# Optimization experiments

Measured on AMD Instinct MI355X. Metric: run time of the kernel, lower is better.

## Reference

```python
import jax, jax.numpy as jnp
import numpy as np

N_NODES = 128
F = 64            # hidden channels (64x0e + 64x1o)
N_RBF = 8
H_R = 64          # radial MLP hidden
L = 2             # num_interactions
R_MAX = 5.0
AVG_NEIGH = 127.0
G_DIM = 16
N_SPECIES = 5

# static fully-connected edge list (no self edges): E = n*(n-1)
_idx = np.arange(N_NODES)
_s, _r = np.meshgrid(_idx, _idx, indexing='ij')
_mask = _s != _r
SENDERS = jnp.asarray(_s[_mask])    # [E]
RECEIVERS = jnp.asarray(_r[_mask])  # [E]


def setup_inputs() -> dict:
    key = jax.random.key(0)
    ks = jax.random.split(key, 12)
    inp = {
        'positions': jax.random.normal(ks[0], (32, N_NODES, 3), jnp.float32),
        'node_features': jax.random.randint(ks[1], (32, N_NODES), 0, N_SPECIES),
        'global_features': jax.random.normal(ks[2], (32, G_DIM), jnp.float32),
        # learned parameters
        'embed': jax.random.normal(ks[3], (N_SPECIES, F), jnp.float32) * 0.1,
        'glob_w': jax.random.normal(ks[4], (G_DIM, F), jnp.float32) * 0.1,
        'rbf_w1': jax.random.normal(ks[5], (L, N_RBF, H_R), jnp.float32) * 0.3,
        'rbf_b1': jnp.zeros((L, H_R), jnp.float32),
        'rbf_w2': jax.random.normal(ks[6], (L, H_R, 3 * F), jnp.float32) * 0.1,
        'ws': jax.random.normal(ks[7], (L, F, F), jnp.float32) * 0.1,
        'wv': jax.random.normal(ks[8], (L, F, F), jnp.float32) * 0.1,
        'wout': jax.random.normal(ks[9], (F,), jnp.float32) * 0.1,
        'final_scaling': jnp.ones((), jnp.float32),
    }
    return inp


def _rbf(d):
    # gaussian radial basis on [0, r_max]
    centers = jnp.linspace(0.0, R_MAX, N_RBF)
    width = R_MAX / N_RBF
    return jnp.exp(-((d[:, None] - centers) ** 2) / (2.0 * width * width))  # [E, N_RBF]


def _single(pos, species, glob, embed, glob_w, rbf_w1, rbf_b1, rbf_w2, ws, wv, wout, final_scaling):
    # graph construction + edge vectors
    edge_vec = pos[RECEIVERS] - pos[SENDERS]                 # [E,3]
    d = jnp.sqrt(jnp.sum(edge_vec ** 2, axis=-1) + 1e-12)   # [E]
    unit = edge_vec / d[:, None]                             # [E,3]
    phi = _rbf(d)                                            # [E,N_RBF]

    # node embedding (species one-hot lookup) conditioned on global features
    s = embed[species] + glob @ glob_w                       # [n,F] scalars
    v = jnp.zeros((N_NODES, F, 3), pos.dtype)                # [n,F,3] vectors

    for l in range(L):
        rw = jax.nn.silu(phi @ rbf_w1[l] + rbf_b1[l]) @ rbf_w2[l]  # [E,3F]
        r1, r2, r3 = jnp.split(rw, 3, axis=-1)               # each [E,F]
        ms = r1 * s[SENDERS]                                 # [E,F]
        mv = r2[..., None] * v[SENDERS] + (r3 * s[SENDERS])[..., None] * unit[:, None, :]  # [E,F,3]
        agg_s = jax.ops.segment_sum(ms, RECEIVERS, num_segments=N_NODES) / AVG_NEIGH
        agg_v = jax.ops.segment_sum(mv, RECEIVERS, num_segments=N_NODES) / AVG_NEIGH
        s = s + agg_s @ ws[l]
        v = v + jnp.einsum('nfd,fg->ngd', agg_v, wv[l])

    out = jnp.einsum('nfd,f->nd', v, wout)                   # equivariant readout [n,3]
    return (out - pos) * final_scaling


def reference(positions, node_features, global_features, embed, glob_w, rbf_w1,
              rbf_b1, rbf_w2, ws, wv, wout, final_scaling):
    fn = lambda p, sp, g: _single(p, sp, g, embed, glob_w, rbf_w1, rbf_b1,
                                  rbf_w2, ws, wv, wout, final_scaling)
    return jax.vmap(fn)(positions, node_features, global_features)
```

## Files before the change

### kernel.cpp

```cpp
#include <hip/hip_runtime.h>
#include <hip/hip_bf16.h>


#define NN 128
#define BB 32
#define FF 64

using f32x4  = __attribute__((ext_vector_type(4))) float;
using short8 = __attribute__((ext_vector_type(8))) short;
using half4  = __attribute__((ext_vector_type(4))) _Float16;

__device__ __forceinline__ unsigned short f2bf(float x) {
    unsigned int u = __float_as_uint(x);
    u += 0x7fff + ((u >> 16) & 1);
    return (unsigned short)(u >> 16);
}
__device__ __forceinline__ unsigned int f2bf_fast32(float x) {
    return (__float_as_uint(x) + 0x8000u) >> 16;
}

__global__ __launch_bounds__(256) void setup_kernel(
    const float* __restrict__ w2,
    const float* __restrict__ ws,
    const float* __restrict__ wv,
    const float* __restrict__ rbf_w1,
    const float* __restrict__ rbf_b1,
    const int* __restrict__ species, const float* __restrict__ glob,
    const float* __restrict__ embed, const float* __restrict__ glob_w,
    short* __restrict__ w2frag,
    float* __restrict__ wT4,
    _Float16* __restrict__ w1A,
    float* __restrict__ s)
{
    const int blk = blockIdx.x;
    if (blk < 192) {
        const int tid = blk * 256 + threadIdx.x;
        const int NFRAG = 24576;
        if (tid < NFRAG) {
            const int e  = tid & 7;
            const int l  = (tid >> 3) & 63;
            const int ks = (tid >> 9) & 1;
            const int q  = tid >> 10;
            const int nt = q % 3;
            const int wv_ = (q / 3) & 3;
            const int layer = q / 12;
            const int col = nt * 64 + wv_ * 16 + (l & 15);
            const int hb  = ks * 32 + (l >> 4) * 8 + e;
            const float val = w2[layer * 64 * 192 + hb * 192 + col] * (1.0f / 127.0f);
            w2frag[tid] = (short)f2bf(val);
        }
        const int tid2 = tid - NFRAG;
        if (tid2 >= 0 && tid2 < 16384) {
            const int c   = tid2 & 3;
            const int g   = (tid2 >> 2) & 63;
            const int ff4 = (tid2 >> 8) & 15;
            const int m   = (tid2 >> 12) & 1;
            const int layer = tid2 >> 13;
            const float* src = (m == 0 ? ws : wv) + layer * 4096;
            wT4[tid2] = src[(ff4 * 4 + c) * 64 + g];
        }
        const int tid3 = tid - NFRAG - 16384;
        if (tid3 >= 0 && tid3 < 2048) {
            const int e  = tid3 & 3;
            const int l  = (tid3 >> 2) & 63;
            const int wv_ = (tid3 >> 8) & 3;
            const int layer = tid3 >> 10;
            const int k = (l >> 4) * 4 + e;
            const int h = wv_ * 16 + (l & 15);
            float val = 0.0f;
            if (k < 8)       val = rbf_w1[layer * 512 + k * 64 + h];
            else if (k == 8) val = rbf_b1[layer * 64 + h];
            w1A[tid3] = (_Float16)val;
        }
    } else {
        const int node = (blk - 192) * 4 + (threadIdx.x >> 6);
        const int b = node >> 7;
        const int f = threadIdx.x & 63;
        const int sp = species[node];
        float acc = embed[sp * FF + f];
#pragma unroll
        for (int k = 0; k < 16; ++k)
            acc = fmaf(glob[b * 16 + k], glob_w[k * FF + f], acc);
        s[node * FF + f] = acc;
    }
}

template<int LAYER>
__global__ __launch_bounds__(256, 4) void msg_kernel(
    const float* __restrict__ pos,
    const float* __restrict__ s_in,
    const float* __restrict__ v_in,
    const half4* __restrict__ w1Abuf,
    const short* __restrict__ w2frag,
    const float* __restrict__ wT4,
    const float* __restrict__ wout,
    const float* __restrict__ scale,
    float* __restrict__ s_out,
    float* __restrict__ v_out,
    float* __restrict__ out)
{
    __shared__ unsigned short hid_lds[NN * 64];
    __shared__ float4 unit_lds[NN];
    __shared__ __align__(16) char phi_pool[NN * 32];
    float4 (*agg4)[16] = (float4(*)[16])phi_pool;

    const int blk = blockIdx.x;
    const int xcd = blk & 7;
    const int idx = blk >> 3;
    const int b = xcd * 4 + (idx >> 7);
    const int i = idx & 127;

    const int t = threadIdx.x;
    const int w = t >> 6;
    const int l = t & 63;
    const int node = b * NN + i;
    const float* pb = pos + b * NN * 3;

    short8 bfrag[3][2];
    {
        const short8* wf = (const short8*)w2frag;
#pragma unroll
        for (int nt = 0; nt < 3; ++nt)
#pragma unroll
            for (int ks = 0; ks < 2; ++ks)
                bfrag[nt][ks] = wf[((w * 3 + nt) * 2 + ks) * 64 + l];
    }

    {
        const int j = t & 127;
        const int half = t >> 7;
        const float dx = pb[i * 3 + 0] - pb[j * 3 + 0];
        const float dy = pb[i * 3 + 1] - pb[j * 3 + 1];
        const float dz = pb[i * 3 + 2] - pb[j * 3 + 2];
        const float d2 = fmaf(dx, dx, fmaf(dy, dy, fmaf(dz, dz, 1e-12f)));
        const float inv = __builtin_amdgcn_rsqf(d2);
        const float dd = d2 * inv;
        if (half == 0)
            unit_lds[j] = make_float4(dx * inv, dy * inv, dz * inv, 0.0f);
        const _Float16 zf = (_Float16)0.f;
        half4 ph;
#pragma unroll
        for (int r = 0; r < 4; ++r) {
            const float td = dd - (float)(half * 4 + r) * (5.0f / 7.0f);
            ph[r] = (_Float16)__expf(td * td * -1.28f);
        }
        if (j == i) ph = (half4){zf, zf, zf, zf};
        char* rowp = phi_pool + j * 32;
        const int swz = ((j >> 2) & 3) << 3;
        *(half4*)(rowp + ((half * 8) ^ swz)) = ph;
        if (half == 0) {
            half4 bias = {(j == i) ? zf : (_Float16)1.0f, zf, zf, zf};
            *(half4*)(rowp + (16 ^ swz)) = bias;
        } else {
            *(half4*)(rowp + (24 ^ swz)) = (half4){zf, zf, zf, zf};
        }
    }
    __syncthreads();

    {
        const half4 w1a = w1Abuf[w * 64 + l];
        const int jcol = l & 15;
        const int chunk = (l >> 4) * 8;
        const int hbyte = w * 32 + (l >> 4) * 8;
#pragma unroll
        for (int mt = 0; mt < 8; ++mt) {
            const int j = mt * 16 + jcol;
            const half4 bphi = *(const half4*)(
                phi_pool + j * 32 + (chunk ^ (((j >> 2) & 3) << 3)));
            f32x4 pre = __builtin_amdgcn_mfma_f32_16x16x16f16(
                w1a, bphi, (f32x4){0.f, 0.f, 0.f, 0.f}, 0, 0, 0);
            unsigned int pk[2];
#pragma unroll
            for (int p = 0; p < 2; ++p) {
                float sv[2];
#pragma unroll
                for (int q = 0; q < 2; ++q) {
                    const float z = pre[p * 2 + q];
                    const float ex = __expf(-z);
                    sv[q] = z * __builtin_amdgcn_rcpf(1.0f + ex);
                }
                pk[p] = f2bf_fast32(sv[0]) | (f2bf_fast32(sv[1]) << 16);
            }
            const int byte = j * 128 + (hbyte ^ ((j & 7) << 4));
            *(uint2*)((char*)hid_lds + byte) = make_uint2(pk[0], pk[1]);
        }
    }
    __syncthreads();

    const int f    = w * 16 + (l & 15);
    const int jsub = (l >> 4) * 4;
    const float* sb = s_in + b * NN * FF;
    const float4* vb4 = (LAYER > 0) ? ((const float4*)v_in) + b * NN * FF : nullptr;

    float accs = 0.f, av0 = 0.f, av1 = 0.f, av2 = 0.f;

    float sP[4]; float4 vP[4];
#pragma unroll
    for (int reg = 0; reg < 4; ++reg) {
        const int j = jsub + reg;
        sP[reg] = sb[j * FF + f];
        if (LAYER > 0) vP[reg] = vb4[j * FF + f];
    }

#pragma unroll
    for (int mt = 0; mt < 8; ++mt) {
        const int jA = mt * 16 + (l & 15);
        const int base = jA * 128;
        const int sw = (jA & 7) << 4;
        const short8 a0 = *(const short8*)((const char*)hid_lds + base + (((l >> 4) * 16 +  0) ^ sw));
        const short8 a1 = *(const short8*)((const char*)hid_lds + base + (((l >> 4) * 16 + 64) ^ sw));

        f32x4 c0 = (f32x4){0.f, 0.f, 0.f, 0.f};
        f32x4 c1 = (f32x4){0.f, 0.f, 0.f, 0.f};
        f32x4 c2 = (f32x4){0.f, 0.f, 0.f, 0.f};
        c0 = __builtin_amdgcn_mfma_f32_16x16x32_bf16(a0, bfrag[0][0], c0, 0, 0, 0);
        c0 = __builtin_amdgcn_mfma_f32_16x16x32_bf16(a1, bfrag[0][1], c0, 0, 0, 0);
        c1 = __builtin_amdgcn_mfma_f32_16x16x32_bf16(a0, bfrag[1][0], c1, 0, 0, 0);
        c1 = __builtin_amdgcn_mfma_f32_16x16x32_bf16(a1, bfrag[1][1], c1, 0, 0, 0);
        c2 = __builtin_amdgcn_mfma_f32_16x16x32_bf16(a0, bfrag[2][0], c2, 0, 0, 0);
        c2 = __builtin_amdgcn_mfma_f32_16x16x32_bf16(a1, bfrag[2][1], c2, 0, 0, 0);

        float sN[4]; float4 vN[4];
        if (mt < 7) {
#pragma unroll
            for (int reg = 0; reg < 4; ++reg) {
                const int j = (mt + 1) * 16 + jsub + reg;
                sN[reg] = sb[j * FF + f];
                if (LAYER > 0) vN[reg] = vb4[j * FF + f];
            }
        }

#pragma unroll
        for (int reg = 0; reg < 4; ++reg) {
            const int j  = mt * 16 + jsub + reg;
            const float r1 = c0[reg];
            const float r2 = c1[reg];
            const float r3 = c2[reg];
            const float sj = sP[reg];
            const float r3s = r3 * sj;
            const float4 u = unit_lds[j];
            accs = fmaf(r1, sj, accs);
            av0 = fmaf(r3s, u.x, av0);
            av1 = fmaf(r3s, u.y, av1);
            av2 = fmaf(r3s, u.z, av2);
            if (LAYER > 0) {
                av0 = fmaf(r2, vP[reg].x, av0);
                av1 = fmaf(r2, vP[reg].y, av1);
                av2 = fmaf(r2, vP[reg].z, av2);
            }
        }
#pragma unroll
        for (int reg = 0; reg < 4; ++reg) {
            sP[reg] = sN[reg];
            if (LAYER > 0) vP[reg] = vN[reg];
        }
    }

    accs += __shfl_xor(accs, 16, 64); accs += __shfl_xor(accs, 32, 64);
    av0  += __shfl_xor(av0, 16, 64);  av0  += __shfl_xor(av0, 32, 64);
    av1  += __shfl_xor(av1, 16, 64);  av1  += __shfl_xor(av1, 32, 64);
    av2  += __shfl_xor(av2, 16, 64);  av2  += __shfl_xor(av2, 32, 64);
    if (l < 16) {
        ((float*)agg4)[0 * 64 + f] = accs;
        ((float*)agg4)[1 * 64 + f] = av0;
        ((float*)agg4)[2 * 64 + f] = av1;
        ((float*)agg4)[3 * 64 + f] = av2;
    }
    __syncthreads();

    const int g = l;
    const float4* wv4 = (const float4*)wT4;
    if (LAYER == 0) {
        const int m = (w == 0) ? 0 : 1;
        const int row = (w == 0) ? 0 : w;
        float a = (w == 0) ? s_in[node * FF + g] : 0.0f;
#pragma unroll
        for (int k = 0; k < 16; ++k) {
            const float4 w4 = wv4[(m * 16 + k) * 64 + g];
            const float4 a4 = agg4[row][k];
            a = fmaf(a4.x, w4.x, a); a = fmaf(a4.y, w4.y, a);
            a = fmaf(a4.z, w4.z, a); a = fmaf(a4.w, w4.w, a);
        }
        if (w == 0) s_out[node * FF + g] = a;
        else        v_out[(node * FF + g) * 4 + (w - 1)] = a;
    } else {
        if (w > 0) {
            const int d = w - 1;
            float a = v_in[(node * FF + g) * 4 + d];
#pragma unroll
            for (int k = 0; k < 16; ++k) {
                const float4 w4 = wv4[(16 + k) * 64 + g];
                const float4 a4 = agg4[w][k];
                a = fmaf(a4.x, w4.x, a); a = fmaf(a4.y, w4.y, a);
                a = fmaf(a4.z, w4.z, a); a = fmaf(a4.w, w4.w, a);
            }
            float p = a * wout[g];
#pragma unroll
            for (int off = 1; off < 64; off <<= 1)
                p += __shfl_xor(p, off, 64);
            if (l == 0)
                out[node * 3 + d] = (p - pos[node * 3 + d]) * scale[0];
        }
    }
}

extern "C" void kernel_launch(void* const* d_in, const int* in_sizes, int n_in,
                              void* d_out, int out_size, void* d_ws, size_t ws_size,
                              hipStream_t stream) {
    const float* pos     = (const float*)d_in[0];
    const int*   species = (const int*)  d_in[1];
    const float* glob    = (const float*)d_in[2];
    const float* embed   = (const float*)d_in[3];
    const float* glob_w  = (const float*)d_in[4];
    const float* rbf_w1  = (const float*)d_in[5];
    const float* rbf_b1  = (const float*)d_in[6];
    const float* rbf_w2  = (const float*)d_in[7];
    const float* ws      = (const float*)d_in[8];
    const float* wv      = (const float*)d_in[9];
    const float* wout    = (const float*)d_in[10];
    const float* scale   = (const float*)d_in[11];

    float* wsf = (float*)d_ws;
    float* s0     = wsf;
    float* s1     = wsf + 262144;
    float* v1     = wsf + 524288;
    short* w2frag = (short*)(wsf + 1572864);
    float* wT4    = wsf + 1585152;
    _Float16* w1A = (_Float16*)(wsf + 1601536);
    float* outp = (float*)d_out;

    setup_kernel<<<dim3(192 + BB * NN / 4), 256, 0, stream>>>(
        rbf_w2, ws, wv, rbf_w1, rbf_b1, species, glob, embed, glob_w,
        w2frag, wT4, w1A, s0);

    msg_kernel<0><<<dim3(NN * BB), 256, 0, stream>>>(
        pos, s0, nullptr,
        (const half4*)w1A, w2frag, wT4, wout, scale,
        s1, v1, nullptr);

    msg_kernel<1><<<dim3(NN * BB), 256, 0, stream>>>(
        pos, s1, v1,
        (const half4*)(w1A + 1024), w2frag + 12288, wT4 + 8192, wout, scale,
        nullptr, nullptr, outp);
}
```

Measured before the change: 82.81 us.

## Transpose node feature buffers to feature-major layout and vectorize message accumulation

```diff
diff --git a/kernel.cpp b/kernel.cpp
--- a/kernel.cpp
+++ b/kernel.cpp
@@ -75,13 +75,14 @@
     } else {
         const int node = (blk - 192) * 4 + (threadIdx.x >> 6);
         const int b = node >> 7;
+        const int n = node & 127;
         const int f = threadIdx.x & 63;
         const int sp = species[node];
         float acc = embed[sp * FF + f];
 #pragma unroll
         for (int k = 0; k < 16; ++k)
             acc = fmaf(glob[b * 16 + k], glob_w[k * FF + f], acc);
-        s[node * FF + f] = acc;
+        s[b * 8192 + f * 128 + n] = acc;
     }
 }
 
@@ -100,9 +101,11 @@
     float* __restrict__ out)
 {
     __shared__ unsigned short hid_lds[NN * 64];
-    __shared__ float4 unit_lds[NN];
+    __shared__ __align__(16) float ux_lds[NN];
+    __shared__ __align__(16) float uy_lds[NN];
+    __shared__ __align__(16) float uz_lds[NN];
     __shared__ __align__(16) char phi_pool[NN * 32];
-    float4 (*agg4)[16] = (float4(*)[16])phi_pool;
+    f32x4 (*agg4)[16] = (f32x4(*)[16])phi_pool;
 
     const int blk = blockIdx.x;
     const int xcd = blk & 7;
@@ -113,8 +116,20 @@
     const int t = threadIdx.x;
     const int w = t >> 6;
     const int l = t & 63;
-    const int node = b * NN + i;
     const float* pb = pos + b * NN * 3;
+
+    const int f    = w * 16 + (l & 15);
+    const int jsub = (l >> 4) * 4;
+    const float* sbf = s_in + b * 8192 + f * 128;
+    const float* vbf = (LAYER > 0) ? (v_in + b * 24576 + f * 384) : nullptr;
+
+    f32x4 sP = *(const f32x4*)(sbf + jsub);
+    f32x4 vxP, vyP, vzP;
+    if (LAYER > 0) {
+        vxP = *(const f32x4*)(vbf +   0 + jsub);
+        vyP = *(const f32x4*)(vbf + 128 + jsub);
+        vzP = *(const f32x4*)(vbf + 256 + jsub);
+    }
 
     short8 bfrag[3][2];
     {
@@ -135,8 +150,11 @@
         const float d2 = fmaf(dx, dx, fmaf(dy, dy, fmaf(dz, dz, 1e-12f)));
         const float inv = __builtin_amdgcn_rsqf(d2);
         const float dd = d2 * inv;
-        if (half == 0)
-            unit_lds[j] = make_float4(dx * inv, dy * inv, dz * inv, 0.0f);
+        if (half == 0) {
+            ux_lds[j] = dx * inv;
+            uy_lds[j] = dy * inv;
+            uz_lds[j] = dz * inv;
+        }
         const _Float16 zf = (_Float16)0.f;
         half4 ph;
 #pragma unroll
@@ -187,23 +205,14 @@
     }
     __syncthreads();
 
-    const int f    = w * 16 + (l & 15);
-    const int jsub = (l >> 4) * 4;
-    const float* sb = s_in + b * NN * FF;
-    const float4* vb4 = (LAYER > 0) ? ((const float4*)v_in) + b * NN * FF : nullptr;
-
-    float accs = 0.f, av0 = 0.f, av1 = 0.f, av2 = 0.f;
-
-    float sP[4]; float4 vP[4];
-#pragma unroll
-    for (int reg = 0; reg < 4; ++reg) {
-        const int j = jsub + reg;
-        sP[reg] = sb[j * FF + f];
-        if (LAYER > 0) vP[reg] = vb4[j * FF + f];
-    }
+    f32x4 accs4 = (f32x4){0.f, 0.f, 0.f, 0.f};
+    f32x4 av04  = (f32x4){0.f, 0.f, 0.f, 0.f};
+    f32x4 av14  = (f32x4){0.f, 0.f, 0.f, 0.f};
+    f32x4 av24  = (f32x4){0.f, 0.f, 0.f, 0.f};
 
 #pragma unroll
     for (int mt = 0; mt < 8; ++mt) {
+        const int j0 = mt * 16 + jsub;
         const int jA = mt * 16 + (l & 15);
         const int base = jA * 128;
         const int sw = (jA & 7) << 4;
@@ -220,42 +229,39 @@
         c2 = __builtin_amdgcn_mfma_f32_16x16x32_bf16(a0, bfrag[2][0], c2, 0, 0, 0);
         c2 = __builtin_amdgcn_mfma_f32_16x16x32_bf16(a1, bfrag[2][1], c2, 0, 0, 0);
 
-        float sN[4]; float4 vN[4];
+        f32x4 sN, vxN, vyN, vzN;
         if (mt < 7) {
-#pragma unroll
-            for (int reg = 0; reg < 4; ++reg) {
-                const int j = (mt + 1) * 16 + jsub + reg;
-                sN[reg] = sb[j * FF + f];
-                if (LAYER > 0) vN[reg] = vb4[j * FF + f];
+            sN = *(const f32x4*)(sbf + j0 + 16);
+            if (LAYER > 0) {
+                vxN = *(const f32x4*)(vbf +   0 + j0 + 16);
+                vyN = *(const f32x4*)(vbf + 128 + j0 + 16);
+                vzN = *(const f32x4*)(vbf + 256 + j0 + 16);
             }
         }
 
-#pragma unroll
-        for (int reg = 0; reg < 4; ++reg) {
-            const int j  = mt * 16 + jsub + reg;
-            const float r1 = c0[reg];
-            const float r2 = c1[reg];
-            const float r3 = c2[reg];
-            const float sj = sP[reg];
-            const float r3s = r3 * sj;
-            const float4 u = unit_lds[j];
-            accs = fmaf(r1, sj, accs);
-            av0 = fmaf(r3s, u.x, av0);
-            av1 = fmaf(r3s, u.y, av1);
-            av2 = fmaf(r3s, u.z, av2);
-            if (LAYER > 0) {
-                av0 = fmaf(r2, vP[reg].x, av0);
-                av1 = fmaf(r2, vP[reg].y, av1);
-                av2 = fmaf(r2, vP[reg].z, av2);
-            }
-        }
-#pragma unroll
-        for (int reg = 0; reg < 4; ++reg) {
-            sP[reg] = sN[reg];
-            if (LAYER > 0) vP[reg] = vN[reg];
-        }
-    }
-
+        const f32x4 ux4 = *(const f32x4*)(ux_lds + j0);
+        const f32x4 uy4 = *(const f32x4*)(uy_lds + j0);
+        const f32x4 uz4 = *(const f32x4*)(uz_lds + j0);
+
+        accs4 = accs4 + c0 * sP;
+        const f32x4 r3s = c2 * sP;
+        av04 = av04 + r3s * ux4;
+        av14 = av14 + r3s * uy4;
+        av24 = av24 + r3s * uz4;
+        if (LAYER > 0) {
+            av04 = av04 + c1 * vxP;
+            av14 = av14 + c1 * vyP;
+            av24 = av24 + c1 * vzP;
+        }
+
+        sP = sN;
+        if (LAYER > 0) { vxP = vxN; vyP = vyN; vzP = vzN; }
+    }
+
+    float accs = (accs4[0] + accs4[1]) + (accs4[2] + accs4[3]);
+    float av0  = (av04[0] + av04[1]) + (av04[2] + av04[3]);
+    float av1  = (av14[0] + av14[1]) + (av14[2] + av14[3]);
+    float av2  = (av24[0] + av24[1]) + (av24[2] + av24[3]);
     accs += __shfl_xor(accs, 16, 64); accs += __shfl_xor(accs, 32, 64);
     av0  += __shfl_xor(av0, 16, 64);  av0  += __shfl_xor(av0, 32, 64);
     av1  += __shfl_xor(av1, 16, 64);  av1  += __shfl_xor(av1, 32, 64);
@@ -269,31 +275,31 @@
     __syncthreads();
 
     const int g = l;
-    const float4* wv4 = (const float4*)wT4;
+    const int node = b * NN + i;
+    const f32x4* wv4 = (const f32x4*)wT4;
     if (LAYER == 0) {
         const int m = (w == 0) ? 0 : 1;
         const int row = (w == 0) ? 0 : w;
-        float a = (w == 0) ? s_in[node * FF + g] : 0.0f;
-#pragma unroll
-        for (int k = 0; k < 16; ++k) {
-            const float4 w4 = wv4[(m * 16 + k) * 64 + g];
-            const float4 a4 = agg4[row][k];
-            a = fmaf(a4.x, w4.x, a); a = fmaf(a4.y, w4.y, a);
-            a = fmaf(a4.z, w4.z, a); a = fmaf(a4.w, w4.w, a);
-        }
-        if (w == 0) s_out[node * FF + g] = a;
-        else        v_out[(node * FF + g) * 4 + (w - 1)] = a;
+        f32x4 a4 = (f32x4){0.f, 0.f, 0.f, 0.f};
+#pragma unroll
+        for (int k = 0; k < 16; ++k)
+            a4 = a4 + wv4[(m * 16 + k) * 64 + g] * agg4[row][k];
+        float a = (a4[0] + a4[1]) + (a4[2] + a4[3]);
+        if (w == 0) {
+            a += s_in[b * 8192 + g * 128 + i];
+            s_out[b * 8192 + g * 128 + i] = a;
+        } else {
+            v_out[b * 24576 + g * 384 + (w - 1) * 128 + i] = a;
+        }
     } else {
         if (w > 0) {
             const int d = w - 1;
-            float a = v_in[(node * FF + g) * 4 + d];
-#pragma unroll
-            for (int k = 0; k < 16; ++k) {
-                const float4 w4 = wv4[(16 + k) * 64 + g];
-                const float4 a4 = agg4[w][k];
-                a = fmaf(a4.x, w4.x, a); a = fmaf(a4.y, w4.y, a);
-                a = fmaf(a4.z, w4.z, a); a = fmaf(a4.w, w4.w, a);
-            }
+            f32x4 a4 = (f32x4){0.f, 0.f, 0.f, 0.f};
+#pragma unroll
+            for (int k = 0; k < 16; ++k)
+                a4 = a4 + wv4[(16 + k) * 64 + g] * agg4[w][k];
+            float a = (a4[0] + a4[1]) + (a4[2] + a4[3])
+                    + v_in[b * 24576 + g * 384 + d * 128 + i];
             float p = a * wout[g];
 #pragma unroll
             for (int off = 1; off < 64; off <<= 1)
@@ -324,9 +330,9 @@
     float* s0     = wsf;
     float* s1     = wsf + 262144;
     float* v1     = wsf + 524288;
-    short* w2frag = (short*)(wsf + 1572864);
-    float* wT4    = wsf + 1585152;
-    _Float16* w1A = (_Float16*)(wsf + 1601536);
+    short* w2frag = (short*)(wsf + 1310720);
+    float* wT4    = wsf + 1323008;
+    _Float16* w1A = (_Float16*)(wsf + 1339392);
     float* outp = (float*)d_out;
 
     setup_kernel<<<dim3(192 + BB * NN / 4), 256, 0, stream>>>(
```

Measured after the change: 108.4 us, median of 2. 30.9% more time.
